# Performance work log

Measured on AMD Instinct MI355X. Metric: run time of the kernel, lower is better.

## Reference

```python
import jax, jax.numpy as jnp
import numpy as np
from jax import lax

N_NODES = 8192
N_FEAT = 256
N_EDGES = 131072


def _cc_labels(src, dst, n):
    """Weakly-connected-component labels via min-label propagation + pointer jumping.
    Converged label[i] == min node index in i's component (matches scipy's
    first-occurrence labeling order after compaction)."""
    def cond(state):
        return state[1]

    def body(state):
        label, _ = state
        m = jnp.minimum(label[src], label[dst])
        new = label.at[src].min(m).at[dst].min(m)
        new = new[new]  # pointer jump
        return new, jnp.any(new != label)

    label, _ = lax.while_loop(cond, body, (jnp.arange(n, dtype=jnp.int32), jnp.array(True)))
    return label


def setup_inputs() -> dict:
    key = jax.random.key(0)
    k1, k2, k3 = jax.random.split(key, 3)
    x = jax.random.normal(k1, (N_NODES, N_FEAT), dtype=jnp.float32)
    edge_index = jax.random.randint(k2, (2, N_EDGES), 0, N_NODES, dtype=jnp.int32)
    batch = jnp.zeros((N_NODES,), dtype=jnp.int32)
    lin_w = jax.random.normal(k3, (1, 2 * N_FEAT), dtype=jnp.float32) * 0.05
    lin_b = jnp.zeros((1,), dtype=jnp.float32)
    return {"x": x, "edge_index": edge_index, "batch": batch, "lin_w": lin_w, "lin_b": lin_b}


def reference(x, edge_index, batch, lin_w, lin_b):
    n, f = x.shape
    src, dst = edge_index[0], edge_index[1]
    msk = src != dst  # drop self loops (kept in buffer, zeroed via mask for static shapes)
    # undirected: add flipped edges -> 2E directed edges
    src2 = jnp.concatenate([src, dst])
    dst2 = jnp.concatenate([dst, src])
    m2 = jnp.concatenate([msk, msk])
    mf = m2.astype(x.dtype)

    # edge score: Linear(2F,1) on [x[src] || x[dst]] == x@w1 gathered + x@w2 gathered
    w1, w2 = lin_w[0, :f], lin_w[0, f:]
    p1 = x @ w1  # [N]
    p2 = x @ w2  # [N]
    e = jnp.tanh(p1[src2] + p2[dst2] + lin_b[0])  # [2E]

    # contracted edges: score > threshold (0.0); masked edges excluded
    contract = m2 & (e > 0.0)
    srcc = jnp.where(contract, src2, 0)
    dstc = jnp.where(contract, dst2, 0)
    label = _cc_labels(srcc, dstc, n)
    # compact labels in order of smallest node index per component (== scipy ordering)
    is_root = (label == jnp.arange(n, dtype=label.dtype))
    cluster = (jnp.cumsum(is_root.astype(jnp.int32)) - 1)[label]  # [N], values in [0, K)

    # dense adjacency A and score adjacency S (scatter-add, like to_dense_adj)
    A = jnp.zeros((n, n), x.dtype).at[src2, dst2].add(mf)
    S = jnp.zeros((n, n), x.dtype).at[src2, dst2].add(e * mf)

    # isolated nodes w.r.t. contracted adjacency -> S[i,i] = 1
    cint = contract.astype(jnp.int32)
    deg = jnp.zeros(n, jnp.int32).at[src2].add(cint) + jnp.zeros(n, jnp.int32).at[dst2].add(cint)
    isolated = deg == 0
    idx = jnp.arange(n)
    S = S.at[idx, idx].set(jnp.where(isolated, jnp.ones((), x.dtype), S[idx, idx]))

    # X_new = (S @ C).T @ X = C.T @ (S.T @ X)  -- C.T@ is a segment-sum over clusters
    # (padded to N rows; rows >= num_clusters are zero)
    X_new = jax.ops.segment_sum(S.T @ x, cluster, num_segments=n)

    # coarsened adjacency C.T @ A @ C with zero diagonal (dense, padded to NxN)
    M1 = jax.ops.segment_sum(A, cluster, num_segments=n)        # pool rows
    A_c = jax.ops.segment_sum(M1.T, cluster, num_segments=n).T  # pool cols
    A_c = A_c.at[idx, idx].set(0.0)

    new_batch = jnp.zeros(n, batch.dtype).at[cluster].set(batch)
    return X_new, A_c, new_batch, cluster
```

## Files before the change

### kernel.cpp

```cpp
#include <hip/hip_runtime.h>
#include <math.h>

#define N_NODES 8192
#define N_FEAT  256
#define N_EDGES 131072
#define N_DIR   (2*N_EDGES)


__device__ __forceinline__ void edge_sd(const int* __restrict__ ei, int k, int& s, int& d){
  s = ei[k];
  d = (k < N_EDGES) ? ei[k + N_EDGES] : ei[k - N_EDGES];
}

__device__ __forceinline__ int rep_lds(int v, int* L){
  int curr = L[v];
  if (curr != v){
    int prev = v, next;
    while (curr > (next = L[curr])){
      L[prev] = next;
      prev = curr;
      curr = next;
    }
  }
  return curr;
}


__global__ void k_zero(uint4* __restrict__ p, long long n4){
  long long i = (long long)blockIdx.x * blockDim.x + threadIdx.x;
  long long stride = (long long)gridDim.x * blockDim.x;
  uint4 z = {0u, 0u, 0u, 0u};
  for (; i < n4; i += stride) p[i] = z;
}

__global__ void k_init(int* __restrict__ cnt, int* __restrict__ deg, int* __restrict__ np){
  int i = blockIdx.x * blockDim.x + threadIdx.x;
  if (i < N_NODES){ cnt[i] = 0; deg[i] = 0; }
  if (i == 0) *np = 0;
}

__global__ void k_proj(const float* __restrict__ x, const float* __restrict__ w,
                       float* __restrict__ p1, float* __restrict__ p2){
  int i = blockIdx.x;
  int t = threadIdx.x;
  float v = x[(size_t)i * N_FEAT + t];
  double a = (double)v * (double)w[t];
  double b = (double)v * (double)w[N_FEAT + t];
  for (int off = 32; off; off >>= 1){
    a += __shfl_down(a, off);
    b += __shfl_down(b, off);
  }
  __shared__ double sa[4], sb[4];
  int wid = t >> 6, lane = t & 63;
  if (lane == 0){ sa[wid] = a; sb[wid] = b; }
  __syncthreads();
  if (t == 0){
    p1[i] = (float)(sa[0] + sa[1] + sa[2] + sa[3]);
    p2[i] = (float)(sb[0] + sb[1] + sb[2] + sb[3]);
  }
}

__global__ void k_edges(const int* __restrict__ ei, const float* __restrict__ p1,
                        const float* __restrict__ p2, const float* __restrict__ lb,
                        float* __restrict__ e_val, int* __restrict__ cnt,
                        int* __restrict__ deg, unsigned int* __restrict__ pairs,
                        int* __restrict__ np){
  int k = blockIdx.x * blockDim.x + threadIdx.x;
  int s, d; edge_sd(ei, k, s, d);
  bool selfe = (s == d);
  float e = 0.0f;
  if (!selfe){
    float z = p1[s] + p2[d] + lb[0];
    e = tanhf(z);
    e_val[k] = e;
    atomicAdd(&cnt[d], 1);
    if (e > 0.0f){
      atomicAdd(&deg[s], 1);
      atomicAdd(&deg[d], 1);
    }
  }
  bool c = (!selfe) && (e > 0.0f);
  unsigned long long m = __ballot(c);
  if (m){
    int lane = threadIdx.x & 63;
    int leader = __ffsll((unsigned long long)m) - 1;
    int base = 0;
    if (lane == leader) base = atomicAdd(np, __popcll(m));
    base = __shfl(base, leader);
    if (c){
      int prefix = __popcll(m & ((1ull << lane) - 1ull));
      pairs[base + prefix] = ((unsigned int)s << 13) | (unsigned int)d;
    }
  }
}

__global__ void k_scan(const int* __restrict__ cnt, int* __restrict__ row_start,
                       int* __restrict__ cursor){
  __shared__ int wsum[1024];
  int t = threadIdx.x;
  int base = t * 8;
  int f[8]; int s = 0;
  #pragma unroll
  for (int j = 0; j < 8; ++j){ f[j] = cnt[base + j]; s += f[j]; }
  wsum[t] = s;
  __syncthreads();
  for (int off = 1; off < 1024; off <<= 1){
    int v = (t >= off) ? wsum[t - off] : 0;
    __syncthreads();
    wsum[t] += v;
    __syncthreads();
  }
  int run = wsum[t] - s;
  #pragma unroll
  for (int j = 0; j < 8; ++j){
    row_start[base + j] = run;
    cursor[base + j]    = run;
    run += f[j];
  }
  if (t == 1023) row_start[N_NODES] = run;
}

__global__ void k_fill(const int* __restrict__ ei, const float* __restrict__ e_val,
                       int* __restrict__ cursor, int* __restrict__ esrc, float* __restrict__ evs){
  int k = blockIdx.x * blockDim.x + threadIdx.x;
  if (k >= N_DIR) return;
  int s, d; edge_sd(ei, k, s, d);
  if (s == d) return;
  int slot = atomicAdd(&cursor[d], 1);
  esrc[slot] = s;
  evs[slot]  = e_val[k];
}

__global__ void __launch_bounds__(1024) k_cc(
    const unsigned int* __restrict__ pairs, const int* __restrict__ np,
    const int* __restrict__ batch,
    int* __restrict__ cluster_i, float* __restrict__ out_cluster,
    float* __restrict__ out_batch){
  __shared__ int L[N_NODES];
  __shared__ int wsum[1024];
  int t = threadIdx.x;

  for (int i = t; i < N_NODES; i += 1024) L[i] = i;
  __syncthreads();

  int n = *np;
  const int CH = 16384;
  for (int cbase = 0; cbase < n; cbase += CH){
    int lim = (cbase + CH < n) ? (cbase + CH) : n;
    for (int k = cbase + t; k < lim; k += 1024){
      unsigned int p = pairs[k];
      int s = (int)(p >> 13), d = (int)(p & 8191u);
      int a = L[s], b = L[d];
      if (a == b) continue;
      a = rep_lds(s, L);
      b = rep_lds(d, L);
      bool repeat;
      do {
        repeat = false;
        if (a != b){
          int ret;
          if (a < b){
            if ((ret = atomicCAS(&L[b], b, a)) != b){ b = ret; repeat = true; }
          } else {
            if ((ret = atomicCAS(&L[a], a, b)) != a){ a = ret; repeat = true; }
          }
        }
      } while (repeat);
    }
    __syncthreads();
    for (int i = t; i < N_NODES; i += 1024){
      int l = L[i];
      while (true){ int q = L[l]; if (q == l) break; l = q; }
      L[i] = l;
    }
    __syncthreads();
  }

  int base = t * 8;
  int l_reg[8];
  #pragma unroll
  for (int j = 0; j < 8; ++j) l_reg[j] = L[base + j];
  __syncthreads();

  int f[8]; int s = 0;
  #pragma unroll
  for (int j = 0; j < 8; ++j){ f[j] = (l_reg[j] == base + j) ? 1 : 0; s += f[j]; }
  wsum[t] = s;
  __syncthreads();
  for (int off = 1; off < 1024; off <<= 1){
    int v = (t >= off) ? wsum[t - off] : 0;
    __syncthreads();
    wsum[t] += v;
    __syncthreads();
  }
  int run = wsum[t] - s;
  #pragma unroll
  for (int j = 0; j < 8; ++j){
    run += f[j];
    if (f[j]) L[base + j] = run - 1;
  }
  __syncthreads();

  #pragma unroll
  for (int j = 0; j < 8; ++j){
    int i = base + j;
    int c = L[l_reg[j]];
    cluster_i[i] = c;
    out_cluster[i] = (float)c;
    out_batch[c] = (float)batch[i];
  }
}

__global__ void k_y(const float* __restrict__ x, const float* __restrict__ evs,
                    const int* __restrict__ esrc, const int* __restrict__ row_start,
                    const int* __restrict__ deg, float* __restrict__ y){
  int i = blockIdx.x;
  int t = threadIdx.x;
  int a = row_start[i], b = row_start[i + 1];
  float acc = (deg[i] == 0) ? x[(size_t)i * N_FEAT + t] : 0.0f;
  for (int j = a; j < b; ++j){
    acc += evs[j] * x[(size_t)esrc[j] * N_FEAT + t];
  }
  y[(size_t)i * N_FEAT + t] = acc;
}

__global__ void k_xnew(const float* __restrict__ y, const int* __restrict__ cluster_i,
                       float* __restrict__ Xn){
  int t = threadIdx.x;
  int node0 = blockIdx.x * 32;
  float acc = 0.0f;
  int cur = cluster_i[node0];
  for (int j = 0; j < 32; ++j){
    int node = node0 + j;
    int c = cluster_i[node];
    if (c != cur){
      atomicAdd(&Xn[(size_t)cur * N_FEAT + t], acc);
      acc = 0.0f; cur = c;
    }
    acc += y[(size_t)node * N_FEAT + t];
  }
  atomicAdd(&Xn[(size_t)cur * N_FEAT + t], acc);
}

__global__ void k_ac(const int* __restrict__ ei, const int* __restrict__ cluster_i,
                     float* __restrict__ Ac){
  int k = blockIdx.x * blockDim.x + threadIdx.x;
  if (k >= N_DIR) return;
  int s, d; edge_sd(ei, k, s, d);
  if (s == d) return;
  int cs = cluster_i[s], cd = cluster_i[d];
  if (cs != cd) atomicAdd(&Ac[(size_t)cs * N_NODES + cd], 1.0f);
}


extern "C" void kernel_launch(void* const* d_in, const int* in_sizes, int n_in,
                              void* d_out, int out_size, void* d_ws, size_t ws_size,
                              hipStream_t stream){
  const float* x     = (const float*)d_in[0];
  const int*   ei    = (const int*)  d_in[1];
  const int*   batch = (const int*)  d_in[2];
  const float* lw    = (const float*)d_in[3];
  const float* lb    = (const float*)d_in[4];

  float* out = (float*)d_out;
  float* Xn  = out;
  float* Ac  = Xn + (size_t)N_NODES * N_FEAT;
  float* ob  = Ac + (size_t)N_NODES * N_NODES;
  float* oc  = ob + N_NODES;

  char* w = (char*)d_ws;
  float* p1        = (float*)w; w += (size_t)N_NODES * 4;
  float* p2        = (float*)w; w += (size_t)N_NODES * 4;
  float* e_val     = (float*)w; w += (size_t)N_DIR   * 4;
  int*   cnt       = (int*)  w; w += (size_t)N_NODES * 4;
  int*   cursor    = (int*)  w; w += (size_t)N_NODES * 4;
  int*   row_start = (int*)  w; w += (size_t)(N_NODES + 8) * 4;
  int*   deg       = (int*)  w; w += (size_t)N_NODES * 4;
  int*   cluster_i = (int*)  w; w += (size_t)N_NODES * 4;
  int*   esrc      = (int*)  w; w += (size_t)N_DIR   * 4;
  float* evs       = (float*)w; w += (size_t)N_DIR   * 4;
  unsigned int* pairs = (unsigned int*)w; w += (size_t)N_DIR * 4;
  int*   np        = (int*)  w; w += 64;
  float* y         = (float*)w; w += (size_t)N_NODES * N_FEAT * 4;

  long long n4 = (long long)out_size / 4;
  k_zero  <<<4096, 256, 0, stream>>>((uint4*)d_out, n4);

  k_init  <<<(N_NODES + 255) / 256, 256, 0, stream>>>(cnt, deg, np);
  k_proj  <<<N_NODES, 256, 0, stream>>>(x, lw, p1, p2);
  k_edges <<<N_DIR / 256, 256, 0, stream>>>(ei, p1, p2, lb, e_val, cnt, deg, pairs, np);
  k_scan  <<<1, 1024, 0, stream>>>(cnt, row_start, cursor);
  k_fill  <<<N_DIR / 256, 256, 0, stream>>>(ei, e_val, cursor, esrc, evs);
  k_cc    <<<1, 1024, 0, stream>>>(pairs, np, batch, cluster_i, oc, ob);
  k_y     <<<N_NODES, 256, 0, stream>>>(x, evs, esrc, row_start, deg, y);
  k_xnew  <<<N_NODES / 32, 256, 0, stream>>>(y, cluster_i, Xn);
  k_ac    <<<N_DIR / 256, 256, 0, stream>>>(ei, cluster_i, Ac);
}
```

Baseline: 280.2 us.

## Move connected-component union-find from single-block LDS to grid-wide global atomics

Replaces the single-workgroup shared-memory union-find with a kernel spread across 1024 blocks that performs lock-free union with path splitting on a global label array, using relaxed agent-scope atomics. The rank/compaction kernel now loads the global labels and finishes pointer chasing to roots before computing the prefix sum. The goal is to remove the serial bottleneck of running all edge unions on one CU. In exchange, every access now goes to global memory and contends on L2 atomics, and the chunked LDS flattening passes are gone.

```diff
diff --git a/kernel.cpp b/kernel.cpp
--- a/kernel.cpp
+++ b/kernel.cpp
@@ -12,17 +12,11 @@
   d = (k < N_EDGES) ? ei[k + N_EDGES] : ei[k - N_EDGES];
 }
 
-__device__ __forceinline__ int rep_lds(int v, int* L){
-  int curr = L[v];
-  if (curr != v){
-    int prev = v, next;
-    while (curr > (next = L[curr])){
-      L[prev] = next;
-      prev = curr;
-      curr = next;
-    }
-  }
-  return curr;
+__device__ __forceinline__ int aload(int* p){
+  return __hip_atomic_load(p, __ATOMIC_RELAXED, __HIP_MEMORY_SCOPE_AGENT);
+}
+__device__ __forceinline__ void astore(int* p, int v){
+  __hip_atomic_store(p, v, __ATOMIC_RELAXED, __HIP_MEMORY_SCOPE_AGENT);
 }
 
 
@@ -33,9 +27,10 @@
   for (; i < n4; i += stride) p[i] = z;
 }
 
-__global__ void k_init(int* __restrict__ cnt, int* __restrict__ deg, int* __restrict__ np){
+__global__ void k_init(int* __restrict__ cnt, int* __restrict__ deg,
+                       int* __restrict__ np, int* __restrict__ label){
   int i = blockIdx.x * blockDim.x + threadIdx.x;
-  if (i < N_NODES){ cnt[i] = 0; deg[i] = 0; }
+  if (i < N_NODES){ cnt[i] = 0; deg[i] = 0; label[i] = i; }
   if (i == 0) *np = 0;
 }
 
@@ -131,55 +126,60 @@
   evs[slot]  = e_val[k];
 }
 
-__global__ void __launch_bounds__(1024) k_cc(
-    const unsigned int* __restrict__ pairs, const int* __restrict__ np,
-    const int* __restrict__ batch,
+__global__ void k_union_g(const unsigned int* __restrict__ pairs,
+                          const int* __restrict__ np, int* __restrict__ label){
+  int n = *np;
+  int k = blockIdx.x * blockDim.x + threadIdx.x;
+  int stride = gridDim.x * blockDim.x;
+  for (; k < n; k += stride){
+    unsigned int p = pairs[k];
+    int s = (int)(p >> 13), d = (int)(p & 8191u);
+    int ps = aload(&label[s]);
+    int pd = aload(&label[d]);
+    if (ps == pd) continue;
+    int a = s, pa = ps;
+    while (pa != a){
+      int g = aload(&label[pa]);
+      if (g != pa) astore(&label[a], g);
+      a = pa; pa = g;
+    }
+    int b = d, pb = pd;
+    while (pb != b){
+      int g = aload(&label[pb]);
+      if (g != pb) astore(&label[b], g);
+      b = pb; pb = g;
+    }
+    while (a != b){
+      if (a < b){ int t = a; a = b; b = t; }
+      int ret = atomicCAS(&label[a], a, b);
+      if (ret == a) break;
+      a = ret;
+      int q = aload(&label[a]);
+      while (q != a){ a = q; q = aload(&label[a]); }
+      int qb = aload(&label[b]);
+      while (qb != b){ b = qb; qb = aload(&label[b]); }
+    }
+  }
+}
+
+__global__ void __launch_bounds__(1024) k_rank(
+    const int* __restrict__ labelG, const int* __restrict__ batch,
     int* __restrict__ cluster_i, float* __restrict__ out_cluster,
     float* __restrict__ out_batch){
   __shared__ int L[N_NODES];
   __shared__ int wsum[1024];
   int t = threadIdx.x;
-
-  for (int i = t; i < N_NODES; i += 1024) L[i] = i;
-  __syncthreads();
-
-  int n = *np;
-  const int CH = 16384;
-  for (int cbase = 0; cbase < n; cbase += CH){
-    int lim = (cbase + CH < n) ? (cbase + CH) : n;
-    for (int k = cbase + t; k < lim; k += 1024){
-      unsigned int p = pairs[k];
-      int s = (int)(p >> 13), d = (int)(p & 8191u);
-      int a = L[s], b = L[d];
-      if (a == b) continue;
-      a = rep_lds(s, L);
-      b = rep_lds(d, L);
-      bool repeat;
-      do {
-        repeat = false;
-        if (a != b){
-          int ret;
-          if (a < b){
-            if ((ret = atomicCAS(&L[b], b, a)) != b){ b = ret; repeat = true; }
-          } else {
-            if ((ret = atomicCAS(&L[a], a, b)) != a){ a = ret; repeat = true; }
-          }
-        }
-      } while (repeat);
-    }
-    __syncthreads();
-    for (int i = t; i < N_NODES; i += 1024){
-      int l = L[i];
-      while (true){ int q = L[l]; if (q == l) break; l = q; }
-      L[i] = l;
-    }
-    __syncthreads();
-  }
+  for (int i = t; i < N_NODES; i += 1024) L[i] = labelG[i];
+  __syncthreads();
 
   int base = t * 8;
   int l_reg[8];
   #pragma unroll
-  for (int j = 0; j < 8; ++j) l_reg[j] = L[base + j];
+  for (int j = 0; j < 8; ++j){
+    int l = L[base + j];
+    while (true){ int q = L[l]; if (q == l) break; l = q; }
+    l_reg[j] = l;
+  }
   __syncthreads();
 
   int f[8]; int s = 0;
@@ -277,6 +277,7 @@
   int*   row_start = (int*)  w; w += (size_t)(N_NODES + 8) * 4;
   int*   deg       = (int*)  w; w += (size_t)N_NODES * 4;
   int*   cluster_i = (int*)  w; w += (size_t)N_NODES * 4;
+  int*   labelG    = (int*)  w; w += (size_t)N_NODES * 4;
   int*   esrc      = (int*)  w; w += (size_t)N_DIR   * 4;
   float* evs       = (float*)w; w += (size_t)N_DIR   * 4;
   unsigned int* pairs = (unsigned int*)w; w += (size_t)N_DIR * 4;
@@ -286,12 +287,13 @@
   long long n4 = (long long)out_size / 4;
   k_zero  <<<4096, 256, 0, stream>>>((uint4*)d_out, n4);
 
-  k_init  <<<(N_NODES + 255) / 256, 256, 0, stream>>>(cnt, deg, np);
+  k_init  <<<(N_NODES + 255) / 256, 256, 0, stream>>>(cnt, deg, np, labelG);
   k_proj  <<<N_NODES, 256, 0, stream>>>(x, lw, p1, p2);
   k_edges <<<N_DIR / 256, 256, 0, stream>>>(ei, p1, p2, lb, e_val, cnt, deg, pairs, np);
   k_scan  <<<1, 1024, 0, stream>>>(cnt, row_start, cursor);
   k_fill  <<<N_DIR / 256, 256, 0, stream>>>(ei, e_val, cursor, esrc, evs);
-  k_cc    <<<1, 1024, 0, stream>>>(pairs, np, batch, cluster_i, oc, ob);
+  k_union_g<<<1024, 256, 0, stream>>>(pairs, np, labelG);
+  k_rank  <<<1, 1024, 0, stream>>>(labelG, batch, cluster_i, oc, ob);
   k_y     <<<N_NODES, 256, 0, stream>>>(x, evs, esrc, row_start, deg, y);
   k_xnew  <<<N_NODES / 32, 256, 0, stream>>>(y, cluster_i, Xn);
   k_ac    <<<N_DIR / 256, 256, 0, stream>>>(ei, cluster_i, Ac);
```

Measured after the change: 791.4 us. 182% more time.
